# Kernel optimization log

Measured on AMD Instinct MI355X. Metric: run time of the kernel, lower is better.

## Reference

```python
import jax, jax.numpy as jnp
import numpy as np

B, L, E, H = 8, 1024, 768, 12
D = E // H  # 64 head dim


def _layernorm(x, scale, bias, eps=1e-6):
    m = jnp.mean(x, axis=-1, keepdims=True)
    v = jnp.var(x, axis=-1, keepdims=True)
    return (x - m) * jax.lax.rsqrt(v + eps) * scale + bias


def setup_inputs() -> dict:
    key = jax.random.key(0)
    ks = jax.random.split(key, 8)
    s = lambda fan_in: 1.0 / np.sqrt(fan_in)  # lecun-normal-ish init scale
    return {
        "x": jax.random.normal(ks[0], (B, L, E), jnp.float32),
        "ln1_scale": jnp.ones((E,), jnp.float32),
        "ln1_bias": jnp.zeros((E,), jnp.float32),
        "w_qkv": jax.random.normal(ks[1], (E, 3 * E), jnp.float32) * s(E),
        "b_qkv": jnp.zeros((3 * E,), jnp.float32),
        "w_proj": jax.random.normal(ks[2], (E, E), jnp.float32) * s(E),
        "b_proj": jnp.zeros((E,), jnp.float32),
        "ln2_scale": jnp.ones((E,), jnp.float32),
        "ln2_bias": jnp.zeros((E,), jnp.float32),
        "w_fc": jax.random.normal(ks[3], (E, 4 * E), jnp.float32) * s(E),
        "b_fc": jnp.zeros((4 * E,), jnp.float32),
        "w_out": jax.random.normal(ks[4], (4 * E, E), jnp.float32) * s(4 * E),
        "b_out": jnp.zeros((E,), jnp.float32),
    }


def reference(x, ln1_scale, ln1_bias, w_qkv, b_qkv, w_proj, b_proj,
              ln2_scale, ln2_bias, w_fc, b_fc, w_out, b_out):
    # eval mode: train=False (all dropouts are identity), mask_len=None
    b, l, _ = x.shape
    # ---- pre-LN causal self-attention ----
    z = _layernorm(x, ln1_scale, ln1_bias)
    qkv = z @ w_qkv + b_qkv                                   # (B, L, 3E)
    # faithful to source: reshape to (B, L, H, 3D) then split last axis
    qkv = qkv.reshape(b, l, H, 3 * D).transpose(0, 2, 1, 3)   # (B, H, L, 3D)
    q, k, v = jnp.split(qkv, 3, axis=-1)                      # each (B, H, L, D)
    attn = jnp.einsum("bhqd,bhkd->bhqk", q, k) / jnp.sqrt(jnp.float32(D))
    mask = jnp.tri(l, dtype=jnp.float32)                      # causal lower-tri
    attn = jnp.where(mask == 0, -1e18, attn)
    attn = jax.nn.softmax(attn, axis=-1)
    y = jnp.einsum("bhqk,bhkd->bhqd", attn, v)                # (B, H, L, D)
    y = y.transpose(0, 2, 1, 3).reshape(b, l, E)
    y = y @ w_proj + b_proj
    x = x + y  # residual (resid dropout is identity in eval)
    # ---- MLP block ----
    z = _layernorm(x, ln2_scale, ln2_bias)
    z = jax.nn.selu(z @ w_fc + b_fc) @ w_out + b_out
    return x + z
```

## Files before the change

kernel.cpp:

```cpp
#include <hip/hip_runtime.h>
#include <hip/hip_bf16.h>

typedef __attribute__((ext_vector_type(8))) short short8;
typedef __attribute__((ext_vector_type(4))) float f32x4;
typedef __attribute__((ext_vector_type(4))) unsigned short us4;

#define AS1 __attribute__((address_space(1)))
#define AS3 __attribute__((address_space(3)))

__device__ __forceinline__ unsigned short f2bf(float f) {
    unsigned u = __float_as_uint(f);
    u += 0x7fffu + ((u >> 16) & 1u);
    return (unsigned short)(u >> 16);
}

__device__ __forceinline__ void gload16(const void* g, void* l) {
    __builtin_amdgcn_global_load_lds((AS1 void*)(g), (AS3 void*)(l), 16, 0, 0);
}

__global__ __launch_bounds__(256) void wT_kernel(const float* __restrict__ in,
                                                 unsigned short* __restrict__ out,
                                                 int K, int N) {
    __shared__ float tile[32][33];
    int tx = threadIdx.x & 31, ty = threadIdx.x >> 5;
    int bn = blockIdx.x * 32, bk = blockIdx.y * 32;
    #pragma unroll
    for (int i = ty; i < 32; i += 8)
        tile[i][tx] = in[(long)(bk + i) * N + bn + tx];
    __syncthreads();
    #pragma unroll
    for (int i = ty; i < 32; i += 8)
        out[(long)(bn + i) * K + bk + tx] = f2bf(tile[tx][i]);
}

__global__ __launch_bounds__(256) void ln_row(const float* __restrict__ x,
                                              const float* __restrict__ sc,
                                              const float* __restrict__ bi,
                                              unsigned short* __restrict__ z) {
    long row = blockIdx.x;
    const float* xr = x + row * 768;
    int t = threadIdx.x;
    float v0 = xr[t], v1 = xr[t + 256], v2 = xr[t + 512];
    float s = v0 + v1 + v2;
    float ss = v0 * v0 + v1 * v1 + v2 * v2;
    #pragma unroll
    for (int m = 1; m < 64; m <<= 1) { s += __shfl_xor(s, m); ss += __shfl_xor(ss, m); }
    __shared__ float red[8];
    int wid = t >> 6;
    if ((t & 63) == 0) { red[wid] = s; red[4 + wid] = ss; }
    __syncthreads();
    s = red[0] + red[1] + red[2] + red[3];
    ss = red[4] + red[5] + red[6] + red[7];
    float mean = s * (1.f / 768.f);
    float var = fmaxf(ss * (1.f / 768.f) - mean * mean, 0.f);
    float rs = rsqrtf(var + 1e-6f);
    unsigned short* zr = z + row * 768;
    zr[t]       = f2bf((v0 - mean) * rs * sc[t]       + bi[t]);
    zr[t + 256] = f2bf((v1 - mean) * rs * sc[t + 256] + bi[t + 256]);
    zr[t + 512] = f2bf((v2 - mean) * rs * sc[t + 512] + bi[t + 512]);
}

template <int MODE>
__global__ __launch_bounds__(256, 2) void gemm_bf16(
    const unsigned short* __restrict__ A, const unsigned short* __restrict__ Bt,
    const float* __restrict__ bias, const float* __restrict__ resid,
    float* __restrict__ outf, unsigned short* __restrict__ outb,
    unsigned short* __restrict__ vt, int M, int N, int K) {
    __shared__ unsigned short As[128 * 64];
    __shared__ unsigned short Bs[128 * 64];
    const int tid = threadIdx.x, lane = tid & 63, wid = tid >> 6;
    const int wr = wid >> 1, wc = wid & 1;
    const long row0 = (long)blockIdx.y * 128, col0 = (long)blockIdx.x * 128;

    f32x4 acc[4][4] = {};
    const int nkt = K >> 6;
    for (int t = 0; t < nkt; ++t) {
        #pragma unroll
        for (int kq = 0; kq < 4; kq++) {
            int U = kq * 256 + tid;
            int r = U >> 3, ch = U & 7;
            int kb = (ch * 16) ^ ((r & 7) << 4);
            gload16(A + (row0 + r) * K + t * 64 + (kb >> 1), &As[(kq * 256 + wid * 64) * 8]);
            gload16(Bt + (col0 + r) * K + t * 64 + (kb >> 1), &Bs[(kq * 256 + wid * 64) * 8]);
        }
        __syncthreads();
        #pragma unroll
        for (int kk = 0; kk < 2; kk++) {
            short8 af[4], bf[4];
            #pragma unroll
            for (int m = 0; m < 4; m++) {
                int r = wr * 64 + m * 16 + (lane & 15);
                int off = r * 128 + ((kk * 64 + ((lane >> 4) * 16)) ^ ((r & 7) << 4));
                af[m] = *(const short8*)((const char*)As + off);
            }
            #pragma unroll
            for (int n = 0; n < 4; n++) {
                int r = wc * 64 + n * 16 + (lane & 15);
                int off = r * 128 + ((kk * 64 + ((lane >> 4) * 16)) ^ ((r & 7) << 4));
                bf[n] = *(const short8*)((const char*)Bs + off);
            }
            #pragma unroll
            for (int m = 0; m < 4; m++)
                #pragma unroll
                for (int n = 0; n < 4; n++)
                    acc[m][n] = __builtin_amdgcn_mfma_f32_16x16x32_bf16(af[m], bf[n], acc[m][n], 0, 0, 0);
        }
        __syncthreads();
    }

    const float LAM = 1.0507009873554805f, LAMAL = 1.7580993408473766f;
    #pragma unroll
    for (int n = 0; n < 4; n++) {
        int c = (int)col0 + wc * 64 + n * 16 + (lane & 15);
        float bv = bias[c];
        #pragma unroll
        for (int m = 0; m < 4; m++) {
            long r0 = row0 + wr * 64 + m * 16 + ((lane >> 4) * 4);
            f32x4 v = acc[m][n];
            v += bv;
            if (MODE == 0) {
                int h = c / 192, rem = c - h * 192;
                if (rem < 128) {
                    #pragma unroll
                    for (int r = 0; r < 4; r++) outb[(r0 + r) * 2304 + c] = f2bf(v[r]);
                } else {
                    int d = rem - 128;
                    long bb = r0 >> 10, l = r0 & 1023;
                    us4 p;
                    #pragma unroll
                    for (int r = 0; r < 4; r++) p[r] = f2bf(v[r]);
                    *(us4*)(vt + ((bb * 12 + h) * 64 + d) * 1024 + l) = p;
                }
            } else if (MODE == 1) {
                #pragma unroll
                for (int r = 0; r < 4; r++)
                    outf[(r0 + r) * (long)N + c] = v[r] + resid[(r0 + r) * (long)N + c];
            } else if (MODE == 2) {
                #pragma unroll
                for (int r = 0; r < 4; r++) {
                    float s = v[r];
                    s = s > 0.f ? LAM * s : LAMAL * (__expf(s) - 1.f);
                    outb[(r0 + r) * (long)N + c] = f2bf(s);
                }
            }
        }
    }
}

__global__ __launch_bounds__(256, 2) void attn_kernel(const unsigned short* __restrict__ qkv,
                                                      const unsigned short* __restrict__ vt,
                                                      unsigned short* __restrict__ y) {
    __shared__ unsigned short Qs[128 * 64];
    __shared__ unsigned short Ks[64 * 64];
    __shared__ unsigned short Vs[64 * 64];
    __shared__ unsigned short Ps[4][32 * 64];
    const int tid = threadIdx.x, lane = tid & 63, wid = tid >> 6;
    const int bh = blockIdx.x, qt = blockIdx.y;
    const int b = bh / 12, h = bh - b * 12;
    const long qrow0 = (long)b * 1024 + qt * 128;

    const unsigned short* qptr = qkv + qrow0 * 2304 + h * 192;
    #pragma unroll
    for (int kq = 0; kq < 4; kq++) {
        int U = kq * 256 + tid;
        int r = U >> 3, ch = U & 7;
        int kb = (ch * 16) ^ ((r & 7) << 4);
        gload16(qptr + (long)r * 2304 + (kb >> 1), &Qs[(kq * 256 + wid * 64) * 8]);
    }
    __syncthreads();
    short8 qf[2][2];
    #pragma unroll
    for (int m = 0; m < 2; m++)
        #pragma unroll
        for (int kk = 0; kk < 2; kk++) {
            int r = wid * 32 + m * 16 + (lane & 15);
            int off = r * 128 + ((kk * 64 + ((lane >> 4) * 16)) ^ ((r & 7) << 4));
            qf[m][kk] = *(const short8*)((const char*)Qs + off);
        }

    f32x4 O[2][4] = {};
    float mrow[2][4], lrow[2][4];
    #pragma unroll
    for (int m = 0; m < 2; m++)
        #pragma unroll
        for (int r = 0; r < 4; r++) { mrow[m][r] = -3.0e38f; lrow[m][r] = 0.f; }

    const int qlo = qt * 128 + wid * 32;
    const int nkv = (qt + 1) * 2;
    const unsigned short* kptr = qkv + (long)b * 1024 * 2304 + h * 192 + 64;
    const unsigned short* vptr = vt + (long)bh * 64 * 1024;

    for (int kvt = 0; kvt < nkv; ++kvt) {
        #pragma unroll
        for (int kq = 0; kq < 2; kq++) {
            int U = kq * 256 + tid;
            int r = U >> 3, ch = U & 7;
            int kb = (ch * 16) ^ ((r & 7) << 4);
            gload16(kptr + (long)(kvt * 64 + r) * 2304 + (kb >> 1), &Ks[(kq * 256 + wid * 64) * 8]);
            gload16(vptr + (long)r * 1024 + kvt * 64 + (kb >> 1), &Vs[(kq * 256 + wid * 64) * 8]);
        }
        __syncthreads();
        if (kvt * 64 <= qlo + 31) {
            f32x4 s[2][4] = {};
            #pragma unroll
            for (int kk = 0; kk < 2; kk++) {
                short8 kf[4];
                #pragma unroll
                for (int n = 0; n < 4; n++) {
                    int r = n * 16 + (lane & 15);
                    int off = r * 128 + ((kk * 64 + ((lane >> 4) * 16)) ^ ((r & 7) << 4));
                    kf[n] = *(const short8*)((const char*)Ks + off);
                }
                #pragma unroll
                for (int m = 0; m < 2; m++)
                    #pragma unroll
                    for (int n = 0; n < 4; n++)
                        s[m][n] = __builtin_amdgcn_mfma_f32_16x16x32_bf16(qf[m][kk], kf[n], s[m][n], 0, 0, 0);
            }
            const bool needmask = (kvt * 64 + 63) > qlo;
            #pragma unroll
            for (int m = 0; m < 2; m++)
                #pragma unroll
                for (int n = 0; n < 4; n++) {
                    s[m][n] = s[m][n] * 0.125f;
                    if (needmask) {
                        int c = kvt * 64 + n * 16 + (lane & 15);
                        #pragma unroll
                        for (int r = 0; r < 4; r++) {
                            int rr = qlo + m * 16 + ((lane >> 4) * 4) + r;
                            if (c > rr) s[m][n][r] = -1.0e30f;
                        }
                    }
                }
            #pragma unroll
            for (int m = 0; m < 2; m++)
                #pragma unroll
                for (int r = 0; r < 4; r++) {
                    float mx = fmaxf(fmaxf(s[m][0][r], s[m][1][r]), fmaxf(s[m][2][r], s[m][3][r]));
                    #pragma unroll
                    for (int msk = 1; msk < 16; msk <<= 1) mx = fmaxf(mx, __shfl_xor(mx, msk));
                    float mnew = fmaxf(mrow[m][r], mx);
                    float al = __expf(mrow[m][r] - mnew);
                    float ps = 0.f;
                    #pragma unroll
                    for (int n = 0; n < 4; n++) {
                        float p = __expf(s[m][n][r] - mnew);
                        s[m][n][r] = p;
                        ps += p;
                    }
                    #pragma unroll
                    for (int msk = 1; msk < 16; msk <<= 1) ps += __shfl_xor(ps, msk);
                    lrow[m][r] = lrow[m][r] * al + ps;
                    mrow[m][r] = mnew;
                    #pragma unroll
                    for (int n = 0; n < 4; n++) O[m][n][r] *= al;
                }
            unsigned short* pw = Ps[wid];
            #pragma unroll
            for (int m = 0; m < 2; m++)
                #pragma unroll
                for (int n = 0; n < 4; n++)
                    #pragma unroll
                    for (int r = 0; r < 4; r++) {
                        int pr = m * 16 + ((lane >> 4) * 4) + r;
                        int off = (pr * 128 + (n * 16 + (lane & 15)) * 2) ^ ((pr & 7) << 4);
                        *(unsigned short*)((char*)pw + off) = f2bf(s[m][n][r]);
                    }
            #pragma unroll
            for (int kk = 0; kk < 2; kk++) {
                short8 pf[2], vf[4];
                #pragma unroll
                for (int m = 0; m < 2; m++) {
                    int r = m * 16 + (lane & 15);
                    int off = r * 128 + ((kk * 64 + ((lane >> 4) * 16)) ^ ((r & 7) << 4));
                    pf[m] = *(const short8*)((const char*)pw + off);
                }
                #pragma unroll
                for (int n = 0; n < 4; n++) {
                    int r = n * 16 + (lane & 15);
                    int off = r * 128 + ((kk * 64 + ((lane >> 4) * 16)) ^ ((r & 7) << 4));
                    vf[n] = *(const short8*)((const char*)Vs + off);
                }
                #pragma unroll
                for (int m = 0; m < 2; m++)
                    #pragma unroll
                    for (int n = 0; n < 4; n++)
                        O[m][n] = __builtin_amdgcn_mfma_f32_16x16x32_bf16(pf[m], vf[n], O[m][n], 0, 0, 0);
            }
        }
        __syncthreads();
    }
    unsigned short* yb = y + (qrow0 + wid * 32) * 768 + h * 64;
    #pragma unroll
    for (int m = 0; m < 2; m++)
        #pragma unroll
        for (int n = 0; n < 4; n++)
            #pragma unroll
            for (int r = 0; r < 4; r++) {
                int rr = m * 16 + ((lane >> 4) * 4) + r;
                yb[(long)rr * 768 + n * 16 + (lane & 15)] = f2bf(O[m][n][r] / lrow[m][r]);
            }
}

extern "C" void kernel_launch(void* const* d_in, const int* in_sizes, int n_in,
                              void* d_out, int out_size, void* d_ws, size_t ws_size,
                              hipStream_t stream) {
    (void)in_sizes; (void)n_in; (void)out_size; (void)ws_size;
    const float* x      = (const float*)d_in[0];
    const float* ln1_s  = (const float*)d_in[1];
    const float* ln1_b  = (const float*)d_in[2];
    const float* w_qkv  = (const float*)d_in[3];
    const float* b_qkv  = (const float*)d_in[4];
    const float* w_proj = (const float*)d_in[5];
    const float* b_proj = (const float*)d_in[6];
    const float* ln2_s  = (const float*)d_in[7];
    const float* ln2_b  = (const float*)d_in[8];
    const float* w_fc   = (const float*)d_in[9];
    const float* b_fc   = (const float*)d_in[10];
    const float* w_out  = (const float*)d_in[11];
    const float* b_out  = (const float*)d_in[12];

    unsigned short* wqkvT = (unsigned short*)d_ws;
    unsigned short* wprojT = wqkvT + (size_t)2304 * 768;
    unsigned short* wfcT   = wprojT + (size_t)768 * 768;
    unsigned short* woutT  = wfcT + (size_t)3072 * 768;
    unsigned short* zbuf   = woutT + (size_t)768 * 3072;
    unsigned short* qkvb   = zbuf + (size_t)8192 * 768;
    unsigned short* vtb    = qkvb + (size_t)8192 * 2304;
    unsigned short* abuf   = qkvb;
    float* x2 = (float*)(vtb + (size_t)96 * 64 * 1024);

    wT_kernel<<<dim3(72, 24), 256, 0, stream>>>(w_qkv, wqkvT, 768, 2304);
    wT_kernel<<<dim3(24, 24), 256, 0, stream>>>(w_proj, wprojT, 768, 768);
    wT_kernel<<<dim3(96, 24), 256, 0, stream>>>(w_fc, wfcT, 768, 3072);
    wT_kernel<<<dim3(24, 96), 256, 0, stream>>>(w_out, woutT, 3072, 768);

    ln_row<<<8192, 256, 0, stream>>>(x, ln1_s, ln1_b, zbuf);
    gemm_bf16<0><<<dim3(18, 64), 256, 0, stream>>>(zbuf, wqkvT, b_qkv, nullptr, nullptr, qkvb, vtb, 8192, 2304, 768);
    attn_kernel<<<dim3(96, 8), 256, 0, stream>>>(qkvb, vtb, zbuf);
    gemm_bf16<1><<<dim3(6, 64), 256, 0, stream>>>(zbuf, wprojT, b_proj, x, x2, nullptr, nullptr, 8192, 768, 768);
    ln_row<<<8192, 256, 0, stream>>>(x2, ln2_s, ln2_b, zbuf);
    gemm_bf16<2><<<dim3(24, 64), 256, 0, stream>>>(zbuf, wfcT, b_fc, nullptr, nullptr, abuf, nullptr, 8192, 3072, 768);
    gemm_bf16<1><<<dim3(6, 64), 256, 0, stream>>>(abuf, woutT, b_out, x2, (float*)d_out, nullptr, nullptr, 8192, 768, 3072);
}
```

Measured before the change: 423.2 us.

## Pair causal query tiles per block, swizzle GEMM blocks, merge weight transposes

Three changes land together. The four weight-transpose launches become one kernel that picks its matrix from the block index, which saves launch overhead. The GEMM remaps block IDs with a stride-8 swizzle, so the blocks that run at the same time touch different tiles, a scheduling change meant for cache or XCD locality. The attention grid is halved, and each block now processes query tile q and tile 7-q one after the other, which balances the causal work across blocks at the cost of fewer blocks (384) to keep the GPU busy.

```diff
diff --git a/kernel.cpp b/kernel.cpp
--- a/kernel.cpp
+++ b/kernel.cpp
@@ -18,12 +18,22 @@
     __builtin_amdgcn_global_load_lds((AS1 void*)(g), (AS3 void*)(l), 16, 0, 0);
 }
 
-__global__ __launch_bounds__(256) void wT_kernel(const float* __restrict__ in,
-                                                 unsigned short* __restrict__ out,
-                                                 int K, int N) {
+__global__ __launch_bounds__(256) void wT_all(const float* __restrict__ w_qkv,
+                                              const float* __restrict__ w_proj,
+                                              const float* __restrict__ w_fc,
+                                              const float* __restrict__ w_out,
+                                              unsigned short* __restrict__ wqkvT,
+                                              unsigned short* __restrict__ wprojT,
+                                              unsigned short* __restrict__ wfcT,
+                                              unsigned short* __restrict__ woutT) {
     __shared__ float tile[32][33];
+    int id = blockIdx.x;
+    const float* in; unsigned short* out; int K, N, bn, bk;
+    if (id < 1728)      {            in = w_qkv;  out = wqkvT;  K = 768;  N = 2304; bn = (id % 72) * 32; bk = (id / 72) * 32; }
+    else if (id < 2304) { id -= 1728; in = w_proj; out = wprojT; K = 768;  N = 768;  bn = (id % 24) * 32; bk = (id / 24) * 32; }
+    else if (id < 4608) { id -= 2304; in = w_fc;   out = wfcT;   K = 768;  N = 3072; bn = (id % 96) * 32; bk = (id / 96) * 32; }
+    else                { id -= 4608; in = w_out;  out = woutT;  K = 3072; N = 768;  bn = (id % 24) * 32; bk = (id / 24) * 32; }
     int tx = threadIdx.x & 31, ty = threadIdx.x >> 5;
-    int bn = blockIdx.x * 32, bk = blockIdx.y * 32;
     #pragma unroll
     for (int i = ty; i < 32; i += 8)
         tile[i][tx] = in[(long)(bk + i) * N + bn + tx];
@@ -70,7 +80,11 @@
     __shared__ unsigned short Bs[128 * 64];
     const int tid = threadIdx.x, lane = tid & 63, wid = tid >> 6;
     const int wr = wid >> 1, wc = wid & 1;
-    const long row0 = (long)blockIdx.y * 128, col0 = (long)blockIdx.x * 128;
+    const int nwg = gridDim.x * gridDim.y;
+    const int orig = blockIdx.y * gridDim.x + blockIdx.x;
+    const int swz = (orig & 7) * (nwg >> 3) + (orig >> 3);
+    const int bx = swz % gridDim.x, by = swz / gridDim.x;
+    const long row0 = (long)by * 128, col0 = (long)bx * 128;
 
     f32x4 acc[4][4] = {};
     const int nkt = K >> 6;
@@ -155,151 +169,156 @@
     __shared__ unsigned short Vs[64 * 64];
     __shared__ unsigned short Ps[4][32 * 64];
     const int tid = threadIdx.x, lane = tid & 63, wid = tid >> 6;
-    const int bh = blockIdx.x, qt = blockIdx.y;
+    const int bh = blockIdx.x;
     const int b = bh / 12, h = bh - b * 12;
-    const long qrow0 = (long)b * 1024 + qt * 128;
-
-    const unsigned short* qptr = qkv + qrow0 * 2304 + h * 192;
-    #pragma unroll
-    for (int kq = 0; kq < 4; kq++) {
-        int U = kq * 256 + tid;
-        int r = U >> 3, ch = U & 7;
-        int kb = (ch * 16) ^ ((r & 7) << 4);
-        gload16(qptr + (long)r * 2304 + (kb >> 1), &Qs[(kq * 256 + wid * 64) * 8]);
-    }
-    __syncthreads();
-    short8 qf[2][2];
-    #pragma unroll
-    for (int m = 0; m < 2; m++)
-        #pragma unroll
-        for (int kk = 0; kk < 2; kk++) {
-            int r = wid * 32 + m * 16 + (lane & 15);
-            int off = r * 128 + ((kk * 64 + ((lane >> 4) * 16)) ^ ((r & 7) << 4));
-            qf[m][kk] = *(const short8*)((const char*)Qs + off);
-        }
-
-    f32x4 O[2][4] = {};
-    float mrow[2][4], lrow[2][4];
-    #pragma unroll
-    for (int m = 0; m < 2; m++)
-        #pragma unroll
-        for (int r = 0; r < 4; r++) { mrow[m][r] = -3.0e38f; lrow[m][r] = 0.f; }
-
-    const int qlo = qt * 128 + wid * 32;
-    const int nkv = (qt + 1) * 2;
     const unsigned short* kptr = qkv + (long)b * 1024 * 2304 + h * 192 + 64;
     const unsigned short* vptr = vt + (long)bh * 64 * 1024;
 
-    for (int kvt = 0; kvt < nkv; ++kvt) {
-        #pragma unroll
-        for (int kq = 0; kq < 2; kq++) {
+    #pragma unroll
+    for (int qi = 0; qi < 2; qi++) {
+        const int qt = qi ? (7 - (int)blockIdx.y) : (int)blockIdx.y;
+        const long qrow0 = (long)b * 1024 + qt * 128;
+
+        const unsigned short* qptr = qkv + qrow0 * 2304 + h * 192;
+        #pragma unroll
+        for (int kq = 0; kq < 4; kq++) {
             int U = kq * 256 + tid;
             int r = U >> 3, ch = U & 7;
             int kb = (ch * 16) ^ ((r & 7) << 4);
-            gload16(kptr + (long)(kvt * 64 + r) * 2304 + (kb >> 1), &Ks[(kq * 256 + wid * 64) * 8]);
-            gload16(vptr + (long)r * 1024 + kvt * 64 + (kb >> 1), &Vs[(kq * 256 + wid * 64) * 8]);
+            gload16(qptr + (long)r * 2304 + (kb >> 1), &Qs[(kq * 256 + wid * 64) * 8]);
         }
         __syncthreads();
-        if (kvt * 64 <= qlo + 31) {
-            f32x4 s[2][4] = {};
+        short8 qf[2][2];
+        #pragma unroll
+        for (int m = 0; m < 2; m++)
             #pragma unroll
             for (int kk = 0; kk < 2; kk++) {
-                short8 kf[4];
-                #pragma unroll
-                for (int n = 0; n < 4; n++) {
-                    int r = n * 16 + (lane & 15);
-                    int off = r * 128 + ((kk * 64 + ((lane >> 4) * 16)) ^ ((r & 7) << 4));
-                    kf[n] = *(const short8*)((const char*)Ks + off);
-                }
+                int r = wid * 32 + m * 16 + (lane & 15);
+                int off = r * 128 + ((kk * 64 + ((lane >> 4) * 16)) ^ ((r & 7) << 4));
+                qf[m][kk] = *(const short8*)((const char*)Qs + off);
+            }
+
+        f32x4 O[2][4] = {};
+        float mrow[2][4], lrow[2][4];
+        #pragma unroll
+        for (int m = 0; m < 2; m++)
+            #pragma unroll
+            for (int r = 0; r < 4; r++) { mrow[m][r] = -3.0e38f; lrow[m][r] = 0.f; }
+
+        const int qlo = qt * 128 + wid * 32;
+        const int nkv = (qt + 1) * 2;
+
+        for (int kvt = 0; kvt < nkv; ++kvt) {
+            #pragma unroll
+            for (int kq = 0; kq < 2; kq++) {
+                int U = kq * 256 + tid;
+                int r = U >> 3, ch = U & 7;
+                int kb = (ch * 16) ^ ((r & 7) << 4);
+                gload16(kptr + (long)(kvt * 64 + r) * 2304 + (kb >> 1), &Ks[(kq * 256 + wid * 64) * 8]);
+                gload16(vptr + (long)r * 1024 + kvt * 64 + (kb >> 1), &Vs[(kq * 256 + wid * 64) * 8]);
+            }
+            __syncthreads();
+            if (kvt * 64 <= qlo + 31) {
+                f32x4 s[2][4] = {};
+                #pragma unroll
+                for (int kk = 0; kk < 2; kk++) {
+                    short8 kf[4];
+                    #pragma unroll
+                    for (int n = 0; n < 4; n++) {
+                        int r = n * 16 + (lane & 15);
+                        int off = r * 128 + ((kk * 64 + ((lane >> 4) * 16)) ^ ((r & 7) << 4));
+                        kf[n] = *(const short8*)((const char*)Ks + off);
+                    }
+                    #pragma unroll
+                    for (int m = 0; m < 2; m++)
+                        #pragma unroll
+                        for (int n = 0; n < 4; n++)
+                            s[m][n] = __builtin_amdgcn_mfma_f32_16x16x32_bf16(qf[m][kk], kf[n], s[m][n], 0, 0, 0);
+                }
+                const bool needmask = (kvt * 64 + 63) > qlo;
                 #pragma unroll
                 for (int m = 0; m < 2; m++)
                     #pragma unroll
+                    for (int n = 0; n < 4; n++) {
+                        s[m][n] = s[m][n] * 0.125f;
+                        if (needmask) {
+                            int c = kvt * 64 + n * 16 + (lane & 15);
+                            #pragma unroll
+                            for (int r = 0; r < 4; r++) {
+                                int rr = qlo + m * 16 + ((lane >> 4) * 4) + r;
+                                if (c > rr) s[m][n][r] = -1.0e30f;
+                            }
+                        }
+                    }
+                #pragma unroll
+                for (int m = 0; m < 2; m++)
+                    #pragma unroll
+                    for (int r = 0; r < 4; r++) {
+                        float mx = fmaxf(fmaxf(s[m][0][r], s[m][1][r]), fmaxf(s[m][2][r], s[m][3][r]));
+                        #pragma unroll
+                        for (int msk = 1; msk < 16; msk <<= 1) mx = fmaxf(mx, __shfl_xor(mx, msk));
+                        float mnew = fmaxf(mrow[m][r], mx);
+                        float al = __expf(mrow[m][r] - mnew);
+                        float ps = 0.f;
+                        #pragma unroll
+                        for (int n = 0; n < 4; n++) {
+                            float p = __expf(s[m][n][r] - mnew);
+                            s[m][n][r] = p;
+                            ps += p;
+                        }
+                        #pragma unroll
+                        for (int msk = 1; msk < 16; msk <<= 1) ps += __shfl_xor(ps, msk);
+                        lrow[m][r] = lrow[m][r] * al + ps;
+                        mrow[m][r] = mnew;
+                        #pragma unroll
+                        for (int n = 0; n < 4; n++) O[m][n][r] *= al;
+                    }
+                unsigned short* pw = Ps[wid];
+                #pragma unroll
+                for (int m = 0; m < 2; m++)
+                    #pragma unroll
                     for (int n = 0; n < 4; n++)
-                        s[m][n] = __builtin_amdgcn_mfma_f32_16x16x32_bf16(qf[m][kk], kf[n], s[m][n], 0, 0, 0);
-            }
-            const bool needmask = (kvt * 64 + 63) > qlo;
-            #pragma unroll
-            for (int m = 0; m < 2; m++)
-                #pragma unroll
-                for (int n = 0; n < 4; n++) {
-                    s[m][n] = s[m][n] * 0.125f;
-                    if (needmask) {
-                        int c = kvt * 64 + n * 16 + (lane & 15);
                         #pragma unroll
                         for (int r = 0; r < 4; r++) {
-                            int rr = qlo + m * 16 + ((lane >> 4) * 4) + r;
-                            if (c > rr) s[m][n][r] = -1.0e30f;
+                            int pr = m * 16 + ((lane >> 4) * 4) + r;
+                            int off = (pr * 128 + (n * 16 + (lane & 15)) * 2) ^ ((pr & 7) << 4);
+                            *(unsigned short*)((char*)pw + off) = f2bf(s[m][n][r]);
                         }
-                    }
-                }
-            #pragma unroll
-            for (int m = 0; m < 2; m++)
+                #pragma unroll
+                for (int kk = 0; kk < 2; kk++) {
+                    short8 pf[2], vf[4];
+                    #pragma unroll
+                    for (int m = 0; m < 2; m++) {
+                        int r = m * 16 + (lane & 15);
+                        int off = r * 128 + ((kk * 64 + ((lane >> 4) * 16)) ^ ((r & 7) << 4));
+                        pf[m] = *(const short8*)((const char*)pw + off);
+                    }
+                    #pragma unroll
+                    for (int n = 0; n < 4; n++) {
+                        int r = n * 16 + (lane & 15);
+                        int off = r * 128 + ((kk * 64 + ((lane >> 4) * 16)) ^ ((r & 7) << 4));
+                        vf[n] = *(const short8*)((const char*)Vs + off);
+                    }
+                    #pragma unroll
+                    for (int m = 0; m < 2; m++)
+                        #pragma unroll
+                        for (int n = 0; n < 4; n++)
+                            O[m][n] = __builtin_amdgcn_mfma_f32_16x16x32_bf16(pf[m], vf[n], O[m][n], 0, 0, 0);
+                }
+            }
+            __syncthreads();
+        }
+        unsigned short* yb = y + (qrow0 + wid * 32) * 768 + h * 64;
+        #pragma unroll
+        for (int m = 0; m < 2; m++)
+            #pragma unroll
+            for (int n = 0; n < 4; n++)
                 #pragma unroll
                 for (int r = 0; r < 4; r++) {
-                    float mx = fmaxf(fmaxf(s[m][0][r], s[m][1][r]), fmaxf(s[m][2][r], s[m][3][r]));
-                    #pragma unroll
-                    for (int msk = 1; msk < 16; msk <<= 1) mx = fmaxf(mx, __shfl_xor(mx, msk));
-                    float mnew = fmaxf(mrow[m][r], mx);
-                    float al = __expf(mrow[m][r] - mnew);
-                    float ps = 0.f;
-                    #pragma unroll
-                    for (int n = 0; n < 4; n++) {
-                        float p = __expf(s[m][n][r] - mnew);
-                        s[m][n][r] = p;
-                        ps += p;
-                    }
-                    #pragma unroll
-                    for (int msk = 1; msk < 16; msk <<= 1) ps += __shfl_xor(ps, msk);
-                    lrow[m][r] = lrow[m][r] * al + ps;
-                    mrow[m][r] = mnew;
-                    #pragma unroll
-                    for (int n = 0; n < 4; n++) O[m][n][r] *= al;
-                }
-            unsigned short* pw = Ps[wid];
-            #pragma unroll
-            for (int m = 0; m < 2; m++)
-                #pragma unroll
-                for (int n = 0; n < 4; n++)
-                    #pragma unroll
-                    for (int r = 0; r < 4; r++) {
-                        int pr = m * 16 + ((lane >> 4) * 4) + r;
-                        int off = (pr * 128 + (n * 16 + (lane & 15)) * 2) ^ ((pr & 7) << 4);
-                        *(unsigned short*)((char*)pw + off) = f2bf(s[m][n][r]);
-                    }
-            #pragma unroll
-            for (int kk = 0; kk < 2; kk++) {
-                short8 pf[2], vf[4];
-                #pragma unroll
-                for (int m = 0; m < 2; m++) {
-                    int r = m * 16 + (lane & 15);
-                    int off = r * 128 + ((kk * 64 + ((lane >> 4) * 16)) ^ ((r & 7) << 4));
-                    pf[m] = *(const short8*)((const char*)pw + off);
-                }
-                #pragma unroll
-                for (int n = 0; n < 4; n++) {
-                    int r = n * 16 + (lane & 15);
-                    int off = r * 128 + ((kk * 64 + ((lane >> 4) * 16)) ^ ((r & 7) << 4));
-                    vf[n] = *(const short8*)((const char*)Vs + off);
-                }
-                #pragma unroll
-                for (int m = 0; m < 2; m++)
-                    #pragma unroll
-                    for (int n = 0; n < 4; n++)
-                        O[m][n] = __builtin_amdgcn_mfma_f32_16x16x32_bf16(pf[m], vf[n], O[m][n], 0, 0, 0);
-            }
-        }
-        __syncthreads();
+                    int rr = m * 16 + ((lane >> 4) * 4) + r;
+                    yb[(long)rr * 768 + n * 16 + (lane & 15)] = f2bf(O[m][n][r] / lrow[m][r]);
+                }
     }
-    unsigned short* yb = y + (qrow0 + wid * 32) * 768 + h * 64;
-    #pragma unroll
-    for (int m = 0; m < 2; m++)
-        #pragma unroll
-        for (int n = 0; n < 4; n++)
-            #pragma unroll
-            for (int r = 0; r < 4; r++) {
-                int rr = m * 16 + ((lane >> 4) * 4) + r;
-                yb[(long)rr * 768 + n * 16 + (lane & 15)] = f2bf(O[m][n][r] / lrow[m][r]);
-            }
 }
 
 extern "C" void kernel_launch(void* const* d_in, const int* in_sizes, int n_in,
@@ -330,14 +349,11 @@
     unsigned short* abuf   = qkvb;
     float* x2 = (float*)(vtb + (size_t)96 * 64 * 1024);
 
-    wT_kernel<<<dim3(72, 24), 256, 0, stream>>>(w_qkv, wqkvT, 768, 2304);
-    wT_kernel<<<dim3(24, 24), 256, 0, stream>>>(w_proj, wprojT, 768, 768);
-    wT_kernel<<<dim3(96, 24), 256, 0, stream>>>(w_fc, wfcT, 768, 3072);
-    wT_kernel<<<dim3(24, 96), 256, 0, stream>>>(w_out, woutT, 3072, 768);
+    wT_all<<<6912, 256, 0, stream>>>(w_qkv, w_proj, w_fc, w_out, wqkvT, wprojT, wfcT, woutT);
 
     ln_row<<<8192, 256, 0, stream>>>(x, ln1_s, ln1_b, zbuf);
     gemm_bf16<0><<<dim3(18, 64), 256, 0, stream>>>(zbuf, wqkvT, b_qkv, nullptr, nullptr, qkvb, vtb, 8192, 2304, 768);
-    attn_kernel<<<dim3(96, 8), 256, 0, stream>>>(qkvb, vtb, zbuf);
+    attn_kernel<<<dim3(96, 4), 256, 0, stream>>>(qkvb, vtb, zbuf);
     gemm_bf16<1><<<dim3(6, 64), 256, 0, stream>>>(zbuf, wprojT, b_proj, x, x2, nullptr, nullptr, 8192, 768, 768);
     ln_row<<<8192, 256, 0, stream>>>(x2, ln2_s, ln2_b, zbuf);
     gemm_bf16<2><<<dim3(24, 64), 256, 0, stream>>>(zbuf, wfcT, b_fc, nullptr, nullptr, abuf, nullptr, 8192, 3072, 768);
```

Measured after the change: 386.8 us. -8.6%, faster.
